# Kernel tuning notes

Measured on AMD Instinct MI355X. Metric: run time of the kernel, lower is better.

## Reference

```python
import jax, jax.numpy as jnp
import numpy as np

NUM_LEVELS = 16
MIN_RES = 16
GROWTH = 1.38
TABLE_SZ = 16384
# Per-level resolutions computed in float64 like torch's python-float b**level
RESOLUTIONS = jnp.asarray(np.floor(MIN_RES * GROWTH ** np.arange(NUM_LEVELS)).astype(np.float32))
# Spatial-hash constants; 2654435761 wraps to int32 like torch's .int() arithmetic
H2 = np.uint32(2654435761).astype(np.int32)
H3 = np.int32(805459861)
# Corner order v0..v7 from get_nearest_vertices_coords: 1 -> use ceil, 0 -> use floor
CORNERS = np.array([[0,0,0],[1,0,0],[1,1,0],[0,1,0],[0,0,1],[1,0,1],[1,1,1],[0,1,1]], dtype=bool)


def setup_inputs() -> dict:
    key = jax.random.key(0)
    kx, kt = jax.random.split(key)
    x = jax.random.uniform(kx, (262144, 3), dtype=jnp.float32)
    # original init: uniform(-1e-4, 1e-4); small-scale random values
    tables = jax.random.normal(kt, (NUM_LEVELS, TABLE_SZ, 2), dtype=jnp.float32) * 1e-4
    return {"x": x, "tables": tables}


def reference(x, tables):
    B = x.shape[0]
    F = tables.shape[-1]
    mask = jnp.asarray(CORNERS)  # [8,3]
    scaled = RESOLUTIONS[:, None, None] * x[None]        # [L,B,3]
    lo = jnp.floor(scaled).astype(jnp.int32)             # [L,B,3]
    hi = jnp.ceil(scaled).astype(jnp.int32)              # [L,B,3]
    verts = jnp.where(mask[None, None], hi[:, :, None, :], lo[:, :, None, :])  # [L,B,8,3]
    vx, vy, vz = verts[..., 0], verts[..., 1], verts[..., 2]
    # int32 spatial hash with wraparound multiply, then python-style mod (non-negative)
    idx = jnp.remainder(vx ^ (H2 * vy) ^ (H3 * vz), TABLE_SZ)  # [L,B,8]
    feats = jax.vmap(lambda t, i: t[i])(tables, idx)           # [L,B,8,F]
    # NOTE: faithful to source: interpolation weights use the UNSCALED position
    w = x - jnp.floor(x)                                       # [B,3]
    # trilinear weight per corner = prod_d (w_d if corner high else 1-w_d)
    cw = jnp.prod(jnp.where(mask[None], w[:, None, :], 1.0 - w[:, None, :]), axis=-1)  # [B,8]
    out = jnp.einsum('lbvf,bv->lbf', feats, cw)                # [L,B,F]
    return jnp.transpose(out, (1, 0, 2)).reshape(B, NUM_LEVELS * F)
```

## Files before the change

kernel.cpp:

```cpp
#include <hip/hip_runtime.h>
#include <hip/hip_fp16.h>
#include <stdint.h>


#define NUM_LEVELS 16
#define TABLE_SZ   16384
#define NCHUNK     32
#define BLOCK      512

__constant__ float RESV[NUM_LEVELS] = {
    16.f, 22.f, 30.f, 42.f, 58.f, 80.f, 110.f, 152.f,
    210.f, 290.f, 400.f, 553.f, 763.f, 1053.f, 1453.f, 2005.f
};

__global__ __launch_bounds__(BLOCK, 4)
void hashenc_lds_kernel(const float* __restrict__ x,
                        const float* __restrict__ tables,
                        float* __restrict__ out,
                        int B, int pts_per_block)
{
    __shared__ __half2 tab[TABLE_SZ];

    const int level = blockIdx.x >> 5;
    const int chunk = blockIdx.x & (NCHUNK - 1);

    {
        const float4* __restrict__ gt4 =
            (const float4*)(tables + (size_t)level * (TABLE_SZ * 2));
        #pragma unroll
        for (int i = threadIdx.x; i < TABLE_SZ / 2; i += BLOCK) {
            float4 v = gt4[i];
            tab[2 * i]     = __floats2half2_rn(v.x, v.y);
            tab[2 * i + 1] = __floats2half2_rn(v.z, v.w);
        }
    }
    __syncthreads();

    const float r = RESV[level];
    int b = chunk * pts_per_block + threadIdx.x;
    const int iters = pts_per_block / BLOCK;

    float px = x[3 * b + 0];
    float py = x[3 * b + 1];
    float pz = x[3 * b + 2];

    for (int k = 0; k < iters; ++k) {
        float npx = px, npy = py, npz = pz;
        int nb = b + BLOCK;
        if (k + 1 < iters) {
            npx = x[3 * nb + 0];
            npy = x[3 * nb + 1];
            npz = x[3 * nb + 2];
        }

        float wx = px - floorf(px);
        float wy = py - floorf(py);
        float wz = pz - floorf(pz);
        float ox = 1.f - wx, oy = 1.f - wy, oz = 1.f - wz;

        float cw[8];
        cw[0] = ox * oy * oz;
        cw[1] = wx * oy * oz;
        cw[2] = wx * wy * oz;
        cw[3] = ox * wy * oz;
        cw[4] = ox * oy * wz;
        cw[5] = wx * oy * wz;
        cw[6] = wx * wy * wz;
        cw[7] = ox * wy * wz;

        float sx = r * px, sy = r * py, sz = r * pz;
        uint32_t mxl = ((uint32_t)(int)floorf(sx) & (TABLE_SZ - 1)) << 2;
        uint32_t mxh = ((uint32_t)(int)ceilf(sx)  & (TABLE_SZ - 1)) << 2;
        uint32_t myl = ((2654435761u * (uint32_t)(int)floorf(sy)) & (TABLE_SZ - 1)) << 2;
        uint32_t myh = ((2654435761u * (uint32_t)(int)ceilf(sy))  & (TABLE_SZ - 1)) << 2;
        uint32_t mzl = ((805459861u  * (uint32_t)(int)floorf(sz)) & (TABLE_SZ - 1)) << 2;
        uint32_t mzh = ((805459861u  * (uint32_t)(int)ceilf(sz))  & (TABLE_SZ - 1)) << 2;

        const char* tb = (const char*)tab;
        uint32_t off[8];
        off[0] = mxl ^ myl ^ mzl;
        off[1] = mxh ^ myl ^ mzl;
        off[2] = mxh ^ myh ^ mzl;
        off[3] = mxl ^ myh ^ mzl;
        off[4] = mxl ^ myl ^ mzh;
        off[5] = mxh ^ myl ^ mzh;
        off[6] = mxh ^ myh ^ mzh;
        off[7] = mxl ^ myh ^ mzh;

        float a0 = 0.f, a1 = 0.f;
        #pragma unroll
        for (int c = 0; c < 8; ++c) {
            float2 f = __half22float2(*(const __half2*)(tb + off[c]));
            a0 += f.x * cw[c];
            a1 += f.y * cw[c];
        }

        ((float2*)out)[(size_t)b * NUM_LEVELS + level] = make_float2(a0, a1);

        px = npx; py = npy; pz = npz;
        b = nb;
    }
}

extern "C" void kernel_launch(void* const* d_in, const int* in_sizes, int n_in,
                              void* d_out, int out_size, void* d_ws, size_t ws_size,
                              hipStream_t stream) {
    const float* x      = (const float*)d_in[0];
    const float* tables = (const float*)d_in[1];
    float* out          = (float*)d_out;
    int B = in_sizes[0] / 3;
    int pts_per_block = (B + NCHUNK - 1) / NCHUNK;
    dim3 grid(NUM_LEVELS * NCHUNK);
    hashenc_lds_kernel<<<grid, BLOCK, 0, stream>>>(x, tables, out, B, pts_per_block);
}
```

Baseline: 90.30 us.

## Double block size, use 24-bit hash multiplies, factor corner weights and offsets

Raises the block size to 1024 threads so each block's LDS table fill is amortised over more threads. Each block still handles the same number of points, so it runs half as many loop iterations. Because only the low 14 bits of the hash matter, the full 32-bit multiplies are replaced by __umul24 with the constants' low bits. The xy partial offsets and weights are factored and shared between the two z planes. Two risks come with this: __umul24 keeps only the low 24 bits of the coordinate, which stays exact for these small grid values, and the launch_bounds occupancy hint of 8 may be unattainable with a 32KB LDS table per block.

```diff
diff --git a/kernel.cpp b/kernel.cpp
--- a/kernel.cpp
+++ b/kernel.cpp
@@ -6,14 +6,17 @@
 #define NUM_LEVELS 16
 #define TABLE_SZ   16384
 #define NCHUNK     32
-#define BLOCK      512
+#define BLOCK      1024
 
 __constant__ float RESV[NUM_LEVELS] = {
     16.f, 22.f, 30.f, 42.f, 58.f, 80.f, 110.f, 152.f,
     210.f, 290.f, 400.f, 553.f, 763.f, 1053.f, 1453.f, 2005.f
 };
 
-__global__ __launch_bounds__(BLOCK, 4)
+#define H2_LO 14769u
+#define H3_LO 6037u
+
+__global__ __launch_bounds__(BLOCK, 8)
 void hashenc_lds_kernel(const float* __restrict__ x,
                         const float* __restrict__ tables,
                         float* __restrict__ out,
@@ -58,41 +61,55 @@
         float wz = pz - floorf(pz);
         float ox = 1.f - wx, oy = 1.f - wy, oz = 1.f - wz;
 
-        float cw[8];
-        cw[0] = ox * oy * oz;
-        cw[1] = wx * oy * oz;
-        cw[2] = wx * wy * oz;
-        cw[3] = ox * wy * oz;
-        cw[4] = ox * oy * wz;
-        cw[5] = wx * oy * wz;
-        cw[6] = wx * wy * wz;
-        cw[7] = ox * wy * wz;
-
         float sx = r * px, sy = r * py, sz = r * pz;
         uint32_t mxl = ((uint32_t)(int)floorf(sx) & (TABLE_SZ - 1)) << 2;
         uint32_t mxh = ((uint32_t)(int)ceilf(sx)  & (TABLE_SZ - 1)) << 2;
-        uint32_t myl = ((2654435761u * (uint32_t)(int)floorf(sy)) & (TABLE_SZ - 1)) << 2;
-        uint32_t myh = ((2654435761u * (uint32_t)(int)ceilf(sy))  & (TABLE_SZ - 1)) << 2;
-        uint32_t mzl = ((805459861u  * (uint32_t)(int)floorf(sz)) & (TABLE_SZ - 1)) << 2;
-        uint32_t mzh = ((805459861u  * (uint32_t)(int)ceilf(sz))  & (TABLE_SZ - 1)) << 2;
+        uint32_t myl = (__umul24(H2_LO, (uint32_t)(int)floorf(sy)) & (TABLE_SZ - 1)) << 2;
+        uint32_t myh = (__umul24(H2_LO, (uint32_t)(int)ceilf(sy))  & (TABLE_SZ - 1)) << 2;
+        uint32_t mzl = (__umul24(H3_LO, (uint32_t)(int)floorf(sz)) & (TABLE_SZ - 1)) << 2;
+        uint32_t mzh = (__umul24(H3_LO, (uint32_t)(int)ceilf(sz))  & (TABLE_SZ - 1)) << 2;
+
+        uint32_t oxy0 = mxl ^ myl;
+        uint32_t oxy1 = mxh ^ myl;
+        uint32_t oxy2 = mxh ^ myh;
+        uint32_t oxy3 = mxl ^ myh;
+        float wxy0 = ox * oy;
+        float wxy1 = wx * oy;
+        float wxy2 = wx * wy;
+        float wxy3 = ox * wy;
 
         const char* tb = (const char*)tab;
-        uint32_t off[8];
-        off[0] = mxl ^ myl ^ mzl;
-        off[1] = mxh ^ myl ^ mzl;
-        off[2] = mxh ^ myh ^ mzl;
-        off[3] = mxl ^ myh ^ mzl;
-        off[4] = mxl ^ myl ^ mzh;
-        off[5] = mxh ^ myl ^ mzh;
-        off[6] = mxh ^ myh ^ mzh;
-        off[7] = mxl ^ myh ^ mzh;
+        float a0 = 0.f, a1 = 0.f;
 
-        float a0 = 0.f, a1 = 0.f;
-        #pragma unroll
-        for (int c = 0; c < 8; ++c) {
-            float2 f = __half22float2(*(const __half2*)(tb + off[c]));
-            a0 += f.x * cw[c];
-            a1 += f.y * cw[c];
+        {
+            __half2 h0 = *(const __half2*)(tb + (oxy0 ^ mzl));
+            __half2 h1 = *(const __half2*)(tb + (oxy1 ^ mzl));
+            __half2 h2 = *(const __half2*)(tb + (oxy2 ^ mzl));
+            __half2 h3 = *(const __half2*)(tb + (oxy3 ^ mzl));
+            float w0 = wxy0 * oz, w1 = wxy1 * oz, w2 = wxy2 * oz, w3 = wxy3 * oz;
+            a0 = fmaf(__low2float(h0),  w0, a0);
+            a1 = fmaf(__high2float(h0), w0, a1);
+            a0 = fmaf(__low2float(h1),  w1, a0);
+            a1 = fmaf(__high2float(h1), w1, a1);
+            a0 = fmaf(__low2float(h2),  w2, a0);
+            a1 = fmaf(__high2float(h2), w2, a1);
+            a0 = fmaf(__low2float(h3),  w3, a0);
+            a1 = fmaf(__high2float(h3), w3, a1);
+        }
+        {
+            __half2 h0 = *(const __half2*)(tb + (oxy0 ^ mzh));
+            __half2 h1 = *(const __half2*)(tb + (oxy1 ^ mzh));
+            __half2 h2 = *(const __half2*)(tb + (oxy2 ^ mzh));
+            __half2 h3 = *(const __half2*)(tb + (oxy3 ^ mzh));
+            float w0 = wxy0 * wz, w1 = wxy1 * wz, w2 = wxy2 * wz, w3 = wxy3 * wz;
+            a0 = fmaf(__low2float(h0),  w0, a0);
+            a1 = fmaf(__high2float(h0), w0, a1);
+            a0 = fmaf(__low2float(h1),  w1, a0);
+            a1 = fmaf(__high2float(h1), w1, a1);
+            a0 = fmaf(__low2float(h2),  w2, a0);
+            a1 = fmaf(__high2float(h2), w2, a1);
+            a0 = fmaf(__low2float(h3),  w3, a0);
+            a1 = fmaf(__high2float(h3), w3, a1);
         }
 
         ((float2*)out)[(size_t)b * NUM_LEVELS + level] = make_float2(a0, a1);
```

Result: faster. 87.84 us (-2.7%).
